# Optimization experiments

Measured on AMD Instinct MI355X. Metric: run time of the kernel, lower is better.

Reference implementation:

```python
import jax, jax.numpy as jnp
import numpy as np

GRID = 10          # 10x10 Battleship board -> 100 nodes
HIDDEN = 128
B = 2048
LN_EPS = 1e-5


def _build_grid_edges():
    """Directed 4-neighbor edges on a GRIDxGRID board, with a scalar dir feature."""
    src, dst, ed = [], [], []
    dirs = [(-1, 0), (1, 0), (0, -1), (0, 1)]  # up, down, left, right
    for r in range(GRID):
        for c in range(GRID):
            u = r * GRID + c
            for d, (dr, dc) in enumerate(dirs):
                rr, cc = r + dr, c + dc
                if 0 <= rr < GRID and 0 <= cc < GRID:
                    src.append(u)
                    dst.append(rr * GRID + cc)
                    ed.append(d / 3.0)
    return (np.asarray(src, np.int32), np.asarray(dst, np.int32),
            np.asarray(ed, np.float32)[:, None])


def setup_inputs() -> dict:
    key = jax.random.key(0)
    ks = jax.random.split(key, 8)
    src, dst, ed = _build_grid_edges()  # 360 edges
    H = HIDDEN
    s1 = 1.0 / np.sqrt(H + 1)
    s2 = 1.0 / np.sqrt(H)
    s3 = 1.0 / np.sqrt(2 * H)
    return {
        "x": jax.random.normal(ks[0], (B, GRID * GRID, H), jnp.float32),
        "src_idx": jnp.asarray(src),
        "dst_idx": jnp.asarray(dst),
        "edge_dir": jnp.asarray(ed),
        "w_msg1": jax.random.normal(ks[1], (H + 1, H), jnp.float32) * s1,
        "b_msg1": jnp.zeros((H,), jnp.float32),
        "w_msg2": jax.random.normal(ks[2], (H, H), jnp.float32) * s2,
        "b_msg2": jnp.zeros((H,), jnp.float32),
        "w_upd1": jax.random.normal(ks[3], (2 * H, H), jnp.float32) * s3,
        "b_upd1": jnp.zeros((H,), jnp.float32),
        "w_upd2": jax.random.normal(ks[4], (H, H), jnp.float32) * s2,
        "b_upd2": jnp.zeros((H,), jnp.float32),
        "gamma": jnp.ones((H,), jnp.float32),
        "beta": jnp.zeros((H,), jnp.float32),
    }


def reference(x, src_idx, dst_idx, edge_dir,
              w_msg1, b_msg1, w_msg2, b_msg2,
              w_upd1, b_upd1, w_upd2, b_upd2,
              gamma, beta):
    Bsz, n_nodes, H = x.shape
    E = src_idx.shape[0]
    # gather source node states: [B, E, H]
    x_src = x[:, src_idx, :]
    # edge features broadcast over batch: [B, E, 1]
    ef = jnp.broadcast_to(edge_dir[None], (Bsz, E, edge_dir.shape[-1]))
    # message MLP: Linear -> ReLU -> Linear
    m = jnp.concatenate([x_src, ef], axis=-1)
    m = jax.nn.relu(jnp.einsum('beh,hk->bek', m, w_msg1) + b_msg1)
    messages = jnp.einsum('beh,hk->bek', m, w_msg2) + b_msg2
    # scatter-add aggregate into per-node buffer: [B, N, H]
    agg = jnp.zeros((Bsz, n_nodes, H), x.dtype).at[:, dst_idx, :].add(messages)
    # update MLP on concat([x, agg])
    u = jnp.concatenate([x, agg], axis=-1)
    u = jax.nn.relu(jnp.einsum('bnh,hk->bnk', u, w_upd1) + b_upd1)
    u = jnp.einsum('bnh,hk->bnk', u, w_upd2) + b_upd2
    # residual + LayerNorm
    h = x + u
    mu = jnp.mean(h, axis=-1, keepdims=True)
    var = jnp.mean(jnp.square(h - mu), axis=-1, keepdims=True)
    return (h - mu) * jax.lax.rsqrt(var + LN_EPS) * gamma + beta
```

## Files before the change

kernel.cpp:

```cpp
#include <hip/hip_runtime.h>

#define NNODE 100
#define HDIM  128
#define NEDGE 360
#define NT    512

typedef float f32x4 __attribute__((ext_vector_type(4)));
typedef short s16x8 __attribute__((ext_vector_type(8)));

__device__ __forceinline__ float bf2f(short s) {
  union { unsigned int u; float f; } v;
  v.u = ((unsigned int)(unsigned short)s) << 16;
  return v.f;
}
__device__ __forceinline__ short f2bf(float f) {
  union { float f; unsigned int u; } v; v.f = f;
  unsigned int u = v.u + 0x7fffu + ((v.u >> 16) & 1u);
  return (short)(u >> 16);
}
__device__ __forceinline__ int sidx(int r, int k) {
  return (r << 7) + ((((k >> 3) ^ (r & 15)) << 3) | (k & 7));
}
__device__ __forceinline__ int hidx(int r, int c) {
  return (r << 7) + (c ^ ((r & 4) << 2));
}

__global__ __launch_bounds__(NT)
void prep_all(const float* __restrict__ w_msg1, const float* __restrict__ w_msg2,
              const float* __restrict__ w_upd1, const float* __restrict__ w_upd2,
              const float* __restrict__ b_msg2, const int* __restrict__ dst_idx,
              short* __restrict__ wt, float* __restrict__ bv, int* __restrict__ inl) {
  __shared__ int cnt[NNODE];
  const int bid = blockIdx.x, tid = threadIdx.x;
  if (bid < 96) {
    const int idx = bid * NT + tid;
    const int m = idx >> 14, i = idx & 16383;
    const int n = i >> 7, k = i & 127;
    const float* W = (m == 0) ? w_msg1 : (m == 1) ? w_upd1 : w_upd2;
    const int slot = (m == 0) ? 0 : (m == 1) ? 2 : 3;
    wt[slot * 16384 + n * HDIM + k] = f2bf(W[k * HDIM + n]);
    if (bid == 0) {
      if (tid < NNODE) cnt[tid] = 0;
      __syncthreads();
      if (tid < NEDGE) {
        int d = dst_idx[tid];
        int p = atomicAdd(&cnt[d], 1);
        inl[d * 4 + p] = tid;
      }
      __syncthreads();
      if (tid < NNODE)
        for (int p = cnt[tid]; p < 4; ++p) inl[tid * 4 + p] = -1;
    }
  } else {
    const int u = (bid - 96) * NT + tid;
    const int i = u >> 7, j = u & 127;
    if (i < 128) {
      float s = 0.f;
#pragma unroll 4
      for (int k = 0; k < 128; ++k)
        s += w_msg2[i * HDIM + k] * w_upd1[(HDIM + k) * HDIM + j];
      wt[16384 + j * HDIM + i] = f2bf(s);
    } else if (i == 128) {
      float s = 0.f;
#pragma unroll 4
      for (int k = 0; k < 128; ++k)
        s += b_msg2[k] * w_upd1[(HDIM + k) * HDIM + j];
      bv[j] = s;
    }
  }
}

__global__ __launch_bounds__(NT, 4)
void mpnn_main(const float* __restrict__ x,
               const int* __restrict__ src_idx,
               const float* __restrict__ edge_dir,
               const float* __restrict__ w_msg1,
               const float* __restrict__ b_msg1,
               const float* __restrict__ b_upd1,
               const float* __restrict__ b_upd2,
               const float* __restrict__ gamma,
               const float* __restrict__ beta,
               const short* __restrict__ wt,
               const float* __restrict__ bv_g,
               const int* __restrict__ inl_g,
               float* __restrict__ out)
{
  __shared__ __align__(16) char smem[81744];
  short* bufT = (short*)smem;
  short* bufX = (short*)(smem + 25600);
  short* bufM = (short*)(smem + 51200);
  float* hbuf = (float*)(smem + 25600);
  short* ep   = (short*)(smem + 76800);
  int*   inls = (int*)(smem + 77568);
  float* lnb  = (float*)(smem + 76800);
  float* edv  = (float*)(smem + 79168);
  float* bvs  = (float*)(smem + 79184);
  float* bu1s = (float*)(smem + 79696);
  float* bu2s = (float*)(smem + 80208);
  float* gms  = (float*)(smem + 80720);
  float* bts  = (float*)(smem + 81232);

  const int tid  = threadIdx.x;
  const int lane = tid & 63;
  const int wave = tid >> 6;
  const int quad = lane >> 4;
  const int l16  = lane & 15;
  const int wr   = wave >> 1;
  const int wc   = wave & 1;
  const int b    = blockIdx.x;
  const float* xb = x + (size_t)b * (NNODE * HDIM);

  const int r0 = wr * 32 + l16;
  const int r1 = r0 + 16;
  const int m0 = (r0 < NNODE) ? r0 : 0;
  const int m1 = (r1 < NNODE) ? r1 : 0;

  const int woff = (wc * 64 + l16) * HDIM + quad * 8;

  auto gemm = [&](const short* __restrict__ w, const short* __restrict__ abuf,
                  int ra0, int ra1, f32x4 (&acc)[2][4]) {
    const short* wb = w + woff;
#pragma unroll
    for (int kq = 0; kq < 4; ++kq) {
      const int ko = kq * 32 + quad * 8;
      s16x8 a0 = *(const s16x8*)&abuf[sidx(ra0, ko)];
      s16x8 a1 = *(const s16x8*)&abuf[sidx(ra1, ko)];
#pragma unroll
      for (int ct = 0; ct < 4; ++ct) {
        s16x8 bw = *(const s16x8*)&wb[ct * 16 * HDIM + kq * 32];
        acc[0][ct] = __builtin_amdgcn_mfma_f32_16x16x32_bf16(a0, bw, acc[0][ct], 0, 0, 0);
        acc[1][ct] = __builtin_amdgcn_mfma_f32_16x16x32_bf16(a1, bw, acc[1][ct], 0, 0, 0);
      }
    }
  };

  for (int G = tid; G < NNODE * 16; G += NT) {
    int r = G >> 4, g = G & 15;
    const float4* p = (const float4*)(xb + r * HDIM + g * 8);
    float4 v0 = p[0], v1 = p[1];
    s16x8 h;
    h[0] = f2bf(v0.x); h[1] = f2bf(v0.y); h[2] = f2bf(v0.z); h[3] = f2bf(v0.w);
    h[4] = f2bf(v1.x); h[5] = f2bf(v1.y); h[6] = f2bf(v1.z); h[7] = f2bf(v1.w);
    *(s16x8*)&bufX[sidx(r, g * 8)] = h;
  }
  if (tid < 384) {
    int s = (tid < NEDGE) ? src_idx[tid] : 0;
    float e = (tid < NEDGE) ? edge_dir[tid] : 0.f;
    int d = (int)(e * 3.0f + 0.5f);
    ep[tid] = (short)(s | (d << 7));
    if (tid < NEDGE) edv[d] = e;
  }
  if (tid < NNODE) ((int4*)inls)[tid] = ((const int4*)inl_g)[tid];
  if (tid < HDIM) {
    bvs[tid]  = bv_g[tid];
    bu1s[tid] = b_upd1[tid];
    bu2s[tid] = b_upd2[tid];
    gms[tid]  = gamma[tid];
    bts[tid]  = beta[tid];
  }
  __syncthreads();

  {
    f32x4 acc[2][4] = {};
    gemm(wt, bufX, m0, m1, acc);
#pragma unroll
    for (int rt = 0; rt < 2; ++rt)
#pragma unroll
      for (int i = 0; i < 4; ++i) {
        const int row = wr * 32 + rt * 16 + quad * 4 + i;
        if (row < NNODE) {
#pragma unroll
          for (int ct = 0; ct < 4; ++ct) {
            const int col = wc * 64 + ct * 16 + l16;
            bufT[sidx(row, col)] = f2bf(acc[rt][ct][i]);
          }
        }
      }
  }
  __syncthreads();

  {
    const int ko = (tid & 15) * 8;
    const float4 ba = *(const float4*)&b_msg1[ko];
    const float4 bb = *(const float4*)&b_msg1[ko + 4];
    const float4 wa = *(const float4*)&w_msg1[HDIM * HDIM + ko];
    const float4 wb = *(const float4*)&w_msg1[HDIM * HDIM + ko + 4];
    for (int G = tid; G < NNODE * 16; G += NT) {
      const int v = G >> 4;
      const int4 il = ((const int4*)inls)[v];
      float s[8] = {0, 0, 0, 0, 0, 0, 0, 0};
      const int es[4] = {il.x, il.y, il.z, il.w};
#pragma unroll
      for (int j = 0; j < 4; ++j) {
        if (es[j] >= 0) {
          const int pk = ep[es[j]];
          const float ed = edv[pk >> 7];
          s16x8 t8 = *(const s16x8*)&bufT[sidx(pk & 127, ko)];
          float u;
          u = bf2f(t8[0]) + ba.x + ed * wa.x; s[0] += u > 0.f ? u : 0.f;
          u = bf2f(t8[1]) + ba.y + ed * wa.y; s[1] += u > 0.f ? u : 0.f;
          u = bf2f(t8[2]) + ba.z + ed * wa.z; s[2] += u > 0.f ? u : 0.f;
          u = bf2f(t8[3]) + ba.w + ed * wa.w; s[3] += u > 0.f ? u : 0.f;
          u = bf2f(t8[4]) + bb.x + ed * wb.x; s[4] += u > 0.f ? u : 0.f;
          u = bf2f(t8[5]) + bb.y + ed * wb.y; s[5] += u > 0.f ? u : 0.f;
          u = bf2f(t8[6]) + bb.z + ed * wb.z; s[6] += u > 0.f ? u : 0.f;
          u = bf2f(t8[7]) + bb.w + ed * wb.w; s[7] += u > 0.f ? u : 0.f;
        }
      }
      s16x8 o;
#pragma unroll
      for (int t = 0; t < 8; ++t) o[t] = f2bf(s[t]);
      *(s16x8*)&bufM[sidx(v, ko)] = o;
    }
  }
  __syncthreads();

  {
    f32x4 acc[2][4] = {};
    gemm(wt + 16384,     bufM, m0, m1, acc);
    gemm(wt + 2 * 16384, bufX, m0, m1, acc);
#pragma unroll
    for (int rt = 0; rt < 2; ++rt)
#pragma unroll
      for (int i = 0; i < 4; ++i) {
        const int row = wr * 32 + rt * 16 + quad * 4 + i;
        if (row < NNODE) {
          const int4 il = ((const int4*)inls)[row];
          const float cn = (float)((il.x >= 0) + (il.y >= 0) + (il.z >= 0) + (il.w >= 0));
#pragma unroll
          for (int ct = 0; ct < 4; ++ct) {
            const int col = wc * 64 + ct * 16 + l16;
            float v = acc[rt][ct][i] + bu1s[col] + cn * bvs[col];
            bufT[sidx(row, col)] = f2bf(v > 0.f ? v : 0.f);
          }
        }
      }
  }
  __syncthreads();

  {
    f32x4 acc[2][4] = {};
    gemm(wt + 3 * 16384, bufT, m0, m1, acc);
#pragma unroll
    for (int rt = 0; rt < 2; ++rt)
#pragma unroll
      for (int i = 0; i < 4; ++i) {
        const int row = wr * 32 + rt * 16 + quad * 4 + i;
        if (row < NNODE) {
          float s1 = 0.f, s2 = 0.f;
#pragma unroll
          for (int ct = 0; ct < 4; ++ct) {
            const int col = wc * 64 + ct * 16 + l16;
            const float h = acc[rt][ct][i] + bu2s[col] + xb[row * HDIM + col];
            hbuf[hidx(row, col)] = h;
            s1 += h; s2 += h * h;
          }
#pragma unroll
          for (int off = 8; off > 0; off >>= 1) {
            s1 += __shfl_xor(s1, off, 64);
            s2 += __shfl_xor(s2, off, 64);
          }
          if (l16 == 0) { lnb[row * 4 + wc * 2] = s1; lnb[row * 4 + wc * 2 + 1] = s2; }
        }
      }
    __syncthreads();
    for (int G = tid; G < NNODE * 32; G += NT) {
      const int row = G >> 5;
      const int c = (G & 31) * 4;
      const float4 h = *(const float4*)&hbuf[hidx(row, c)];
      const float s1 = lnb[row * 4] + lnb[row * 4 + 2];
      const float s2 = lnb[row * 4 + 1] + lnb[row * 4 + 3];
      const float mu  = s1 * (1.0f / HDIM);
      const float var = s2 * (1.0f / HDIM) - mu * mu;
      const float rs  = rsqrtf(var + 1e-5f);
      const float4 g  = *(const float4*)&gms[c];
      const float4 bt = *(const float4*)&bts[c];
      float4 o;
      o.x = (h.x - mu) * rs * g.x + bt.x;
      o.y = (h.y - mu) * rs * g.y + bt.y;
      o.z = (h.z - mu) * rs * g.z + bt.z;
      o.w = (h.w - mu) * rs * g.w + bt.w;
      *(float4*)&out[((size_t)b * NNODE + row) * HDIM + c] = o;
    }
  }
}

extern "C" void kernel_launch(void* const* d_in, const int* in_sizes, int n_in,
                              void* d_out, int out_size, void* d_ws, size_t ws_size,
                              hipStream_t stream) {
  const float* x      = (const float*)d_in[0];
  const int*   src    = (const int*)  d_in[1];
  const int*   dst    = (const int*)  d_in[2];
  const float* ed     = (const float*)d_in[3];
  const float* w_msg1 = (const float*)d_in[4];
  const float* b_msg1 = (const float*)d_in[5];
  const float* w_msg2 = (const float*)d_in[6];
  const float* b_msg2 = (const float*)d_in[7];
  const float* w_upd1 = (const float*)d_in[8];
  const float* b_upd1 = (const float*)d_in[9];
  const float* w_upd2 = (const float*)d_in[10];
  const float* b_upd2 = (const float*)d_in[11];
  const float* gamma  = (const float*)d_in[12];
  const float* beta   = (const float*)d_in[13];
  float* out = (float*)d_out;

  short* wt  = (short*)d_ws;
  float* bv  = (float*)((char*)d_ws + 131072);
  int*   inl = (int*)((char*)d_ws + 131584);

  prep_all<<<129, NT, 0, stream>>>(w_msg1, w_msg2, w_upd1, w_upd2, b_msg2,
                                   dst, wt, bv, inl);

  const int Bsz = in_sizes[0] / (NNODE * HDIM);
  mpnn_main<<<Bsz, NT, 0, stream>>>(x, src, ed, w_msg1, b_msg1,
                                    b_upd1, b_upd2, gamma, beta, wt, bv, inl, out);
}
```

Before: 350.2 us.

## Fuse message aggregation into update GEMM and remap waves to full-width row tiles

```diff
diff --git a/kernel.cpp b/kernel.cpp
--- a/kernel.cpp
+++ b/kernel.cpp
@@ -70,7 +70,7 @@
   }
 }
 
-__global__ __launch_bounds__(NT, 4)
+__global__ __launch_bounds__(NT, 6)
 void mpnn_main(const float* __restrict__ x,
                const int* __restrict__ src_idx,
                const float* __restrict__ edge_dir,
@@ -85,54 +85,26 @@
                const int* __restrict__ inl_g,
                float* __restrict__ out)
 {
-  __shared__ __align__(16) char smem[81744];
-  short* bufT = (short*)smem;
-  short* bufX = (short*)(smem + 25600);
-  short* bufM = (short*)(smem + 51200);
-  float* hbuf = (float*)(smem + 25600);
-  short* ep   = (short*)(smem + 76800);
-  int*   inls = (int*)(smem + 77568);
-  float* lnb  = (float*)(smem + 76800);
-  float* edv  = (float*)(smem + 79168);
-  float* bvs  = (float*)(smem + 79184);
-  float* bu1s = (float*)(smem + 79696);
-  float* bu2s = (float*)(smem + 80208);
-  float* gms  = (float*)(smem + 80720);
-  float* bts  = (float*)(smem + 81232);
+  __shared__ __align__(16) char smem[53584];
+  short* bufA = (short*)smem;
+  short* bufB = (short*)(smem + 25600);
+  float* hbuf = (float*)smem;
+  short* ep   = (short*)(smem + 51200);
+  int*   inls = (int*)(smem + 51968);
+  float* edv  = (float*)(smem + 53568);
 
   const int tid  = threadIdx.x;
   const int lane = tid & 63;
-  const int wave = tid >> 6;
+  const int w    = tid >> 6;
   const int quad = lane >> 4;
   const int l16  = lane & 15;
-  const int wr   = wave >> 1;
-  const int wc   = wave & 1;
   const int b    = blockIdx.x;
   const float* xb = x + (size_t)b * (NNODE * HDIM);
 
-  const int r0 = wr * 32 + l16;
-  const int r1 = r0 + 16;
+  const int r0 = w * 16 + l16;
   const int m0 = (r0 < NNODE) ? r0 : 0;
-  const int m1 = (r1 < NNODE) ? r1 : 0;
-
-  const int woff = (wc * 64 + l16) * HDIM + quad * 8;
-
-  auto gemm = [&](const short* __restrict__ w, const short* __restrict__ abuf,
-                  int ra0, int ra1, f32x4 (&acc)[2][4]) {
-    const short* wb = w + woff;
-#pragma unroll
-    for (int kq = 0; kq < 4; ++kq) {
-      const int ko = kq * 32 + quad * 8;
-      s16x8 a0 = *(const s16x8*)&abuf[sidx(ra0, ko)];
-      s16x8 a1 = *(const s16x8*)&abuf[sidx(ra1, ko)];
-#pragma unroll
-      for (int ct = 0; ct < 4; ++ct) {
-        s16x8 bw = *(const s16x8*)&wb[ct * 16 * HDIM + kq * 32];
-        acc[0][ct] = __builtin_amdgcn_mfma_f32_16x16x32_bf16(a0, bw, acc[0][ct], 0, 0, 0);
-        acc[1][ct] = __builtin_amdgcn_mfma_f32_16x16x32_bf16(a1, bw, acc[1][ct], 0, 0, 0);
-      }
-    }
-  };
+
+  const int woff = l16 * HDIM + quad * 8;
 
   for (int G = tid; G < NNODE * 16; G += NT) {
     int r = G >> 4, g = G & 15;
@@ -141,7 +113,7 @@
     s16x8 h;
     h[0] = f2bf(v0.x); h[1] = f2bf(v0.y); h[2] = f2bf(v0.z); h[3] = f2bf(v0.w);
     h[4] = f2bf(v1.x); h[5] = f2bf(v1.y); h[6] = f2bf(v1.z); h[7] = f2bf(v1.w);
-    *(s16x8*)&bufX[sidx(r, g * 8)] = h;
+    *(s16x8*)&bufA[sidx(r, g * 8)] = h;
   }
   if (tid < 384) {
     int s = (tid < NEDGE) ? src_idx[tid] : 0;
@@ -151,43 +123,46 @@
     if (tid < NEDGE) edv[d] = e;
   }
   if (tid < NNODE) ((int4*)inls)[tid] = ((const int4*)inl_g)[tid];
-  if (tid < HDIM) {
-    bvs[tid]  = bv_g[tid];
-    bu1s[tid] = b_upd1[tid];
-    bu2s[tid] = b_upd2[tid];
-    gms[tid]  = gamma[tid];
-    bts[tid]  = beta[tid];
-  }
   __syncthreads();
 
   {
-    f32x4 acc[2][4] = {};
-    gemm(wt, bufX, m0, m1, acc);
-#pragma unroll
-    for (int rt = 0; rt < 2; ++rt)
-#pragma unroll
-      for (int i = 0; i < 4; ++i) {
-        const int row = wr * 32 + rt * 16 + quad * 4 + i;
-        if (row < NNODE) {
-#pragma unroll
-          for (int ct = 0; ct < 4; ++ct) {
-            const int col = wc * 64 + ct * 16 + l16;
-            bufT[sidx(row, col)] = f2bf(acc[rt][ct][i]);
-          }
-        }
-      }
+    f32x4 acc[8] = {};
+    const short* wb = wt + woff;
+#pragma unroll
+    for (int kq = 0; kq < 4; ++kq) {
+      const int ko = kq * 32 + quad * 8;
+      s16x8 a = *(const s16x8*)&bufA[sidx(m0, ko)];
+#pragma unroll
+      for (int ct = 0; ct < 8; ++ct) {
+        s16x8 bw = *(const s16x8*)&wb[ct * 16 * HDIM + kq * 32];
+        acc[ct] = __builtin_amdgcn_mfma_f32_16x16x32_bf16(a, bw, acc[ct], 0, 0, 0);
+      }
+    }
+#pragma unroll
+    for (int i = 0; i < 4; ++i) {
+      const int row = w * 16 + quad * 4 + i;
+      if (row < NNODE) {
+#pragma unroll
+        for (int ct = 0; ct < 8; ++ct) {
+          const int col = ct * 16 + l16;
+          bufB[sidx(row, col)] = f2bf(acc[ct][i] + b_msg1[col]);
+        }
+      }
+    }
   }
   __syncthreads();
 
   {
-    const int ko = (tid & 15) * 8;
-    const float4 ba = *(const float4*)&b_msg1[ko];
-    const float4 bb = *(const float4*)&b_msg1[ko + 4];
-    const float4 wa = *(const float4*)&w_msg1[HDIM * HDIM + ko];
-    const float4 wb = *(const float4*)&w_msg1[HDIM * HDIM + ko + 4];
-    for (int G = tid; G < NNODE * 16; G += NT) {
-      const int v = G >> 4;
-      const int4 il = ((const int4*)inls)[v];
+    f32x4 acc[8] = {};
+    const short* wbC = wt + 16384 + woff;
+    const short* wbU = wt + 2 * 16384 + woff;
+    const int4 il = ((const int4*)inls)[m0];
+#pragma unroll
+    for (int kq = 0; kq < 4; ++kq) {
+      const int ko = kq * 32 + quad * 8;
+      s16x8 a = *(const s16x8*)&bufA[sidx(m0, ko)];
+      const float4 wl0 = *(const float4*)&w_msg1[HDIM * HDIM + ko];
+      const float4 wl1 = *(const float4*)&w_msg1[HDIM * HDIM + ko + 4];
       float s[8] = {0, 0, 0, 0, 0, 0, 0, 0};
       const int es[4] = {il.x, il.y, il.z, il.w};
 #pragma unroll
@@ -195,92 +170,94 @@
         if (es[j] >= 0) {
           const int pk = ep[es[j]];
           const float ed = edv[pk >> 7];
-          s16x8 t8 = *(const s16x8*)&bufT[sidx(pk & 127, ko)];
+          s16x8 t8 = *(const s16x8*)&bufB[sidx(pk & 127, ko)];
           float u;
-          u = bf2f(t8[0]) + ba.x + ed * wa.x; s[0] += u > 0.f ? u : 0.f;
-          u = bf2f(t8[1]) + ba.y + ed * wa.y; s[1] += u > 0.f ? u : 0.f;
-          u = bf2f(t8[2]) + ba.z + ed * wa.z; s[2] += u > 0.f ? u : 0.f;
-          u = bf2f(t8[3]) + ba.w + ed * wa.w; s[3] += u > 0.f ? u : 0.f;
-          u = bf2f(t8[4]) + bb.x + ed * wb.x; s[4] += u > 0.f ? u : 0.f;
-          u = bf2f(t8[5]) + bb.y + ed * wb.y; s[5] += u > 0.f ? u : 0.f;
-          u = bf2f(t8[6]) + bb.z + ed * wb.z; s[6] += u > 0.f ? u : 0.f;
-          u = bf2f(t8[7]) + bb.w + ed * wb.w; s[7] += u > 0.f ? u : 0.f;
-        }
-      }
-      s16x8 o;
-#pragma unroll
-      for (int t = 0; t < 8; ++t) o[t] = f2bf(s[t]);
-      *(s16x8*)&bufM[sidx(v, ko)] = o;
+          u = bf2f(t8[0]) + ed * wl0.x; s[0] += u > 0.f ? u : 0.f;
+          u = bf2f(t8[1]) + ed * wl0.y; s[1] += u > 0.f ? u : 0.f;
+          u = bf2f(t8[2]) + ed * wl0.z; s[2] += u > 0.f ? u : 0.f;
+          u = bf2f(t8[3]) + ed * wl0.w; s[3] += u > 0.f ? u : 0.f;
+          u = bf2f(t8[4]) + ed * wl1.x; s[4] += u > 0.f ? u : 0.f;
+          u = bf2f(t8[5]) + ed * wl1.y; s[5] += u > 0.f ? u : 0.f;
+          u = bf2f(t8[6]) + ed * wl1.z; s[6] += u > 0.f ? u : 0.f;
+          u = bf2f(t8[7]) + ed * wl1.w; s[7] += u > 0.f ? u : 0.f;
+        }
+      }
+      s16x8 mf;
+#pragma unroll
+      for (int t = 0; t < 8; ++t) mf[t] = f2bf(s[t]);
+#pragma unroll
+      for (int ct = 0; ct < 8; ++ct) {
+        s16x8 bwC = *(const s16x8*)&wbC[ct * 16 * HDIM + kq * 32];
+        acc[ct] = __builtin_amdgcn_mfma_f32_16x16x32_bf16(mf, bwC, acc[ct], 0, 0, 0);
+        s16x8 bwU = *(const s16x8*)&wbU[ct * 16 * HDIM + kq * 32];
+        acc[ct] = __builtin_amdgcn_mfma_f32_16x16x32_bf16(a, bwU, acc[ct], 0, 0, 0);
+      }
+    }
+    __syncthreads();
+#pragma unroll
+    for (int i = 0; i < 4; ++i) {
+      const int row = w * 16 + quad * 4 + i;
+      if (row < NNODE) {
+        const int4 il2 = ((const int4*)inls)[row];
+        const float cn = (float)((il2.x >= 0) + (il2.y >= 0) + (il2.z >= 0) + (il2.w >= 0));
+#pragma unroll
+        for (int ct = 0; ct < 8; ++ct) {
+          const int col = ct * 16 + l16;
+          float v = acc[ct][i] + b_upd1[col] + cn * bv_g[col];
+          bufB[sidx(row, col)] = f2bf(v > 0.f ? v : 0.f);
+        }
+      }
     }
   }
   __syncthreads();
 
   {
-    f32x4 acc[2][4] = {};
-    gemm(wt + 16384,     bufM, m0, m1, acc);
-    gemm(wt + 2 * 16384, bufX, m0, m1, acc);
-#pragma unroll
-    for (int rt = 0; rt < 2; ++rt)
-#pragma unroll
-      for (int i = 0; i < 4; ++i) {
-        const int row = wr * 32 + rt * 16 + quad * 4 + i;
-        if (row < NNODE) {
-          const int4 il = ((const int4*)inls)[row];
-          const float cn = (float)((il.x >= 0) + (il.y >= 0) + (il.z >= 0) + (il.w >= 0));
-#pragma unroll
-          for (int ct = 0; ct < 4; ++ct) {
-            const int col = wc * 64 + ct * 16 + l16;
-            float v = acc[rt][ct][i] + bu1s[col] + cn * bvs[col];
-            bufT[sidx(row, col)] = f2bf(v > 0.f ? v : 0.f);
-          }
-        }
-      }
-  }
-  __syncthreads();
-
-  {
-    f32x4 acc[2][4] = {};
-    gemm(wt + 3 * 16384, bufT, m0, m1, acc);
-#pragma unroll
-    for (int rt = 0; rt < 2; ++rt)
-#pragma unroll
-      for (int i = 0; i < 4; ++i) {
-        const int row = wr * 32 + rt * 16 + quad * 4 + i;
-        if (row < NNODE) {
-          float s1 = 0.f, s2 = 0.f;
-#pragma unroll
-          for (int ct = 0; ct < 4; ++ct) {
-            const int col = wc * 64 + ct * 16 + l16;
-            const float h = acc[rt][ct][i] + bu2s[col] + xb[row * HDIM + col];
-            hbuf[hidx(row, col)] = h;
-            s1 += h; s2 += h * h;
-          }
-#pragma unroll
-          for (int off = 8; off > 0; off >>= 1) {
-            s1 += __shfl_xor(s1, off, 64);
-            s2 += __shfl_xor(s2, off, 64);
-          }
-          if (l16 == 0) { lnb[row * 4 + wc * 2] = s1; lnb[row * 4 + wc * 2 + 1] = s2; }
-        }
-      }
+    f32x4 acc[8] = {};
+    const short* wb2 = wt + 3 * 16384 + woff;
+#pragma unroll
+    for (int kq = 0; kq < 4; ++kq) {
+      const int ko = kq * 32 + quad * 8;
+      s16x8 a = *(const s16x8*)&bufB[sidx(m0, ko)];
+#pragma unroll
+      for (int ct = 0; ct < 8; ++ct) {
+        s16x8 bw = *(const s16x8*)&wb2[ct * 16 * HDIM + kq * 32];
+        acc[ct] = __builtin_amdgcn_mfma_f32_16x16x32_bf16(a, bw, acc[ct], 0, 0, 0);
+      }
+    }
+    __syncthreads();
+#pragma unroll
+    for (int i = 0; i < 4; ++i) {
+      const int row = w * 16 + quad * 4 + i;
+      if (row < NNODE) {
+        float h[8];
+        float s1 = 0.f, s2 = 0.f;
+#pragma unroll
+        for (int ct = 0; ct < 8; ++ct) {
+          const int col = ct * 16 + l16;
+          h[ct] = acc[ct][i] + b_upd2[col] + xb[row * HDIM + col];
+          s1 += h[ct]; s2 += h[ct] * h[ct];
+        }
+#pragma unroll
+        for (int off = 8; off > 0; off >>= 1) {
+          s1 += __shfl_xor(s1, off, 64);
+          s2 += __shfl_xor(s2, off, 64);
+        }
+        const float mu  = s1 * (1.0f / HDIM);
+        const float var = s2 * (1.0f / HDIM) - mu * mu;
+        const float rs  = rsqrtf(var + 1e-5f);
+#pragma unroll
+        for (int ct = 0; ct < 8; ++ct) {
+          const int col = ct * 16 + l16;
+          hbuf[hidx(row, col)] = (h[ct] - mu) * rs * gamma[col] + beta[col];
+        }
+      }
+    }
     __syncthreads();
     for (int G = tid; G < NNODE * 32; G += NT) {
       const int row = G >> 5;
       const int c = (G & 31) * 4;
-      const float4 h = *(const float4*)&hbuf[hidx(row, c)];
-      const float s1 = lnb[row * 4] + lnb[row * 4 + 2];
-      const float s2 = lnb[row * 4 + 1] + lnb[row * 4 + 3];
-      const float mu  = s1 * (1.0f / HDIM);
-      const float var = s2 * (1.0f / HDIM) - mu * mu;
-      const float rs  = rsqrtf(var + 1e-5f);
-      const float4 g  = *(const float4*)&gms[c];
-      const float4 bt = *(const float4*)&bts[c];
-      float4 o;
-      o.x = (h.x - mu) * rs * g.x + bt.x;
-      o.y = (h.y - mu) * rs * g.y + bt.y;
-      o.z = (h.z - mu) * rs * g.z + bt.z;
-      o.w = (h.w - mu) * rs * g.w + bt.w;
-      *(float4*)&out[((size_t)b * NNODE + row) * HDIM + c] = o;
+      const float4 v = *(const float4*)&hbuf[hidx(row, c)];
+      *(float4*)&out[((size_t)b * NNODE + row) * HDIM + c] = v;
     }
   }
 }
```

New measurement: 495.7 us. 1.42x slower.
